# Optimization experiments

Measured on AMD Instinct MI355X. Metric: run time of the kernel, lower is better.

## Reference

```python
import jax, jax.numpy as jnp
import numpy as np

B, S, H = 4, 2048, 1024
NH, HD = 16, 64
ROPE_THETA = 160000.0
SCALE = HD ** -0.5


def _rope_cos_sin(position_ids, dim, theta):
    # neox-style rotary: frequencies over half the head dim
    inv_freq = 1.0 / (theta ** (jnp.arange(0, dim, 2, dtype=jnp.float32) / dim))  # [dim/2]
    freqs = position_ids.astype(jnp.float32)[..., None] * inv_freq  # [B,S,dim/2]
    return jnp.cos(freqs), jnp.sin(freqs)


def _apply_rope(x, cos, sin):
    # x: [B,S,NH,HD]; neox style: rotate halves
    d2 = x.shape[-1] // 2
    x1, x2 = x[..., :d2], x[..., d2:]
    c = cos[:, :, None, :]
    s = sin[:, :, None, :]
    return jnp.concatenate([x1 * c - x2 * s, x2 * c + x1 * s], axis=-1)


def setup_inputs() -> dict:
    key = jax.random.key(0)
    k1, k2, k3 = jax.random.split(key, 3)
    hidden_states = jax.random.normal(k1, (B, S, H), dtype=jnp.float32)
    position_ids = jnp.tile(jnp.arange(S, dtype=jnp.int32)[None, :], (B, 1))
    Wqkv = jax.random.normal(k2, (3 * H, H), dtype=jnp.float32) * (H ** -0.5)
    Wo = jax.random.normal(k3, (H, H), dtype=jnp.float32) * (H ** -0.5)
    return {"hidden_states": hidden_states, "position_ids": position_ids,
            "Wqkv": Wqkv, "Wo": Wo}


def reference(hidden_states, position_ids, Wqkv, Wo):
    # fused QKV projection
    qkv = jnp.einsum('bsh,oh->bso', hidden_states, Wqkv)  # [B,S,3H]
    q, k, v = jnp.split(qkv, 3, axis=-1)
    q = q.reshape(B, S, NH, HD)
    k = k.reshape(B, S, NH, HD)
    v = v.reshape(B, S, NH, HD)
    # rotary embedding (neox style)
    cos, sin = _rope_cos_sin(position_ids, HD, ROPE_THETA)
    q = _apply_rope(q, cos, sin)
    k = _apply_rope(k, cos, sin)
    # full bidirectional (encoder-only, global layer) attention
    scores = jnp.einsum('bqhd,bkhd->bhqk', q, k) * SCALE  # [B,NH,S,S]
    probs = jax.nn.softmax(scores, axis=-1)
    ctx = jnp.einsum('bhqk,bkhd->bqhd', probs, v).reshape(B, S, H)
    # output projection
    return jnp.einsum('bsh,oh->bso', ctx, Wo)
```

## Files before the change

### kernel.cpp

```cpp
#include <hip/hip_runtime.h>
#include <hip/hip_bf16.h>


#define GLOBAL_AS __attribute__((address_space(1)))
#define LDS_AS    __attribute__((address_space(3)))

using f32x4  = __attribute__((ext_vector_type(4))) float;
using f32x16 = __attribute__((ext_vector_type(16))) float;
using s16x8  = __attribute__((ext_vector_type(8))) short;

__device__ __forceinline__ void gld_lds16(const void* g, void* l) {
  __builtin_amdgcn_global_load_lds((const GLOBAL_AS void*)g, (LDS_AS void*)l, 16, 0, 0);
}

__device__ __forceinline__ unsigned short f2bf(float f) {
  unsigned int u = __float_as_uint(f);
  u = (u + 0x7fffu + ((u >> 16) & 1u)) >> 16;
  return (unsigned short)u;
}
__device__ __forceinline__ unsigned int cvt_pk_bf16(float lo, float hi) {
  unsigned int r;
  asm("v_cvt_pk_bf16_f32 %0, %1, %2" : "=v"(r) : "v"(lo), "v"(hi));
  return r;
}
__device__ __forceinline__ void pswap(unsigned int& a, unsigned int& b) {
  asm("v_permlane32_swap_b32 %0, %1" : "+v"(a), "+v"(b));
}

__global__ __launch_bounds__(256) void cvt_all_kernel(const float* __restrict__ h,
                                                      const float* __restrict__ wq,
                                                      const float* __restrict__ wo,
                                                      unsigned short* __restrict__ hb,
                                                      unsigned short* __restrict__ wqb,
                                                      unsigned short* __restrict__ wob) {
  int b = blockIdx.x;
  const float* src; unsigned short* dst; int i;
  if (b < 8192)       { src = h;  dst = hb;  i = b * 256 + threadIdx.x; }
  else if (b < 11264) { src = wq; dst = wqb; i = (b - 8192) * 256 + threadIdx.x; }
  else                { src = wo; dst = wob; i = (b - 11264) * 256 + threadIdx.x; }
  float4 v = ((const float4*)src)[i];
  ushort4 o;
  o.x = f2bf(v.x); o.y = f2bf(v.y); o.z = f2bf(v.z); o.w = f2bf(v.w);
  ((ushort4*)dst)[i] = o;
}

__global__ __launch_bounds__(256) void rope_table_kernel(const int* __restrict__ pos,
                                                         float* __restrict__ ctab,
                                                         float* __restrict__ stab) {
  int idx = blockIdx.x * 256 + threadIdx.x;
  int d = idx & 31;
  int bs = idx >> 5;
  float p = (float)pos[bs];
  float inv = exp2f(-(float)d * 0.5402410118609203f);
  float f = p * inv;
  ctab[idx] = cosf(f);
  stab[idx] = sinf(f);
}

template<int MODE>
__global__ __launch_bounds__(256) void gemm_bt_kernel(const unsigned short* __restrict__ A,
                                                      const unsigned short* __restrict__ Bm,
                                                      void* __restrict__ C, int N, int K,
                                                      const float* __restrict__ ctab,
                                                      const float* __restrict__ stab,
                                                      unsigned short* __restrict__ Qr,
                                                      unsigned short* __restrict__ Kr,
                                                      unsigned short* __restrict__ vbuf) {
  __shared__ char sA[16384];
  __shared__ char sB[16384];
  const int tid  = threadIdx.x;
  const int lane = tid & 63, w = tid >> 6;
  const int g = lane >> 4, c = lane & 15;
  const int wr = w >> 1, wc = w & 1;
  const int m0 = blockIdx.x * 128, n0 = blockIdx.y * 128;
  const char* Ab = (const char*)A;
  const char* Bb = (const char*)Bm;

  f32x4 acc[4][4] = {};
  for (int k0 = 0; k0 < K; k0 += 64) {
    __syncthreads();
#pragma unroll
    for (int rr = 0; rr < 4; ++rr) {
      int o = tid * 16 + rr * 4096;
      int row = o >> 7;
      int col = (o & 127) ^ ((row & 7) << 4);
      gld_lds16(Ab + ((size_t)(m0 + row) * K + k0) * 2 + col, sA + o);
      gld_lds16(Bb + ((size_t)(n0 + row) * K + k0) * 2 + col, sB + o);
    }
    __syncthreads();
#pragma unroll
    for (int ks = 0; ks < 2; ++ks) {
      s16x8 af[4], bfr[4];
#pragma unroll
      for (int i = 0; i < 4; ++i) {
        int row = 64 * wr + 16 * i + c;
        af[i] = *(const s16x8*)(sA + ((row * 128 + ks * 64 + g * 16) ^ ((row & 7) << 4)));
      }
#pragma unroll
      for (int j = 0; j < 4; ++j) {
        int row = 64 * wc + 16 * j + c;
        bfr[j] = *(const s16x8*)(sB + ((row * 128 + ks * 64 + g * 16) ^ ((row & 7) << 4)));
      }
#pragma unroll
      for (int i = 0; i < 4; ++i)
#pragma unroll
        for (int j = 0; j < 4; ++j)
          acc[i][j] = __builtin_amdgcn_mfma_f32_16x16x32_bf16(af[i], bfr[j], acc[i][j], 0, 0, 0);
    }
  }

  if (MODE == 1) {
#pragma unroll
    for (int i = 0; i < 4; ++i)
#pragma unroll
      for (int j = 0; j < 4; ++j)
#pragma unroll
        for (int r = 0; r < 4; ++r) {
          int m = m0 + 64 * wr + 16 * i + 4 * g + r;
          int n = n0 + 64 * wc + 16 * j + c;
          ((float*)C)[(size_t)m * N + n] = acc[i][j][r];
        }
  } else {
    const int t = blockIdx.y;
    if (t < 16) {
      unsigned short* dstb = (t < 8) ? Qr : Kr;
      const float qs = (t < 8) ? 0.18033688011112042f : 1.0f;
      const int h = 2 * (t & 7) + wc;
#pragma unroll
      for (int i = 0; i < 4; ++i)
#pragma unroll
        for (int r = 0; r < 4; ++r) {
          int m = m0 + 64 * wr + 16 * i + 4 * g + r;
          int b = m >> 11, s = m & 2047;
          unsigned short* drow = dstb + ((size_t)(b * 16 + h) * 2048 + s) * 64;
#pragma unroll
          for (int j = 0; j < 2; ++j) {
            int d = 16 * j + c;
            float co = ctab[(size_t)m * 32 + d];
            float si = stab[(size_t)m * 32 + d];
            float x1 = acc[i][j][r], x2 = acc[i][j + 2][r];
            drow[d]      = f2bf((x1 * co - x2 * si) * qs);
            drow[d + 32] = f2bf((x2 * co + x1 * si) * qs);
          }
        }
    } else {
#pragma unroll
      for (int i = 0; i < 4; ++i)
#pragma unroll
        for (int j = 0; j < 4; ++j)
#pragma unroll
          for (int r = 0; r < 4; ++r) {
            int m = m0 + 64 * wr + 16 * i + 4 * g + r;
            int n = (t - 16) * 128 + 64 * wc + 16 * j + c;
            vbuf[(size_t)m * 1024 + n] = f2bf(acc[i][j][r]);
          }
    }
  }
}

__global__ __launch_bounds__(256) void vtrans_kernel(const unsigned short* __restrict__ vbuf,
                                                     unsigned short* __restrict__ Vt) {
  __shared__ unsigned short tile[64][80];
  int bid = blockIdx.x;
  int st = bid & 31, h = (bid >> 5) & 15, b = bid >> 9;
  int s0 = st * 64;
  int t = threadIdx.x;
  {
    int row = t >> 2, part = t & 3;
    const unsigned short* src = vbuf + ((size_t)(b * 2048 + s0 + row)) * 1024 + h * 64 + part * 16;
    uint4 v0 = *(const uint4*)(src);
    uint4 v1 = *(const uint4*)(src + 8);
    *(uint4*)&tile[row][part * 16]     = v0;
    *(uint4*)&tile[row][part * 16 + 8] = v1;
  }
  __syncthreads();
  {
    int d = t >> 2, sp = t & 3;
    unsigned short vals[16];
#pragma unroll
    for (int i = 0; i < 16; ++i) vals[i] = tile[sp * 16 + i][d];
    unsigned short* dst = Vt + ((size_t)(b * 16 + h) * 64 + d) * 2048 + s0 + sp * 16;
    *(uint4*)(dst)     = ((const uint4*)vals)[0];
    *(uint4*)(dst + 8) = ((const uint4*)vals)[1];
  }
}

__global__ __launch_bounds__(256) void attn_kernel(const unsigned short* __restrict__ Q,
                                                   const unsigned short* __restrict__ Kr,
                                                   const unsigned short* __restrict__ Vt,
                                                   unsigned short* __restrict__ Ctx) {
  __shared__ char sK[2][8192];
  __shared__ char sV[2][8192];
  const int tid  = threadIdx.x;
  const int lane = tid & 63, w = tid >> 6;
  const int hi = lane >> 5, ql = lane & 31;
  const int swz = (ql & 7) << 4;
  int lin = blockIdx.x + 16 * blockIdx.y;
  int eff = (lin & 7) * 128 + (lin >> 3);
  const int bh = eff >> 4;
  const int q0 = (eff & 15) * 128;
  const char* kh = (const char*)(Kr + (size_t)bh * 2048 * 64);
  const char* vh = (const char*)(Vt + (size_t)bh * 64 * 2048);

  s16x8 qf[4];
  {
    const char* qrow = (const char*)Q + ((size_t)bh * 2048 + q0 + 32 * w + ql) * 128;
#pragma unroll
    for (int t = 0; t < 4; ++t) qf[t] = *(const s16x8*)(qrow + t * 32 + hi * 16);
  }

#pragma unroll
  for (int rr = 0; rr < 2; ++rr) {
    int o = tid * 16 + rr * 4096;
    int l = o ^ (((o >> 7) & 7) << 4);
    gld_lds16(kh + l, sK[0] + o);
    gld_lds16(vh + (size_t)(o >> 7) * 4096 + (l & 127), sV[0] + o);
  }

  float l_run = 0.f;
  f32x16 oa0 = {}, oa1 = {};

  for (int it = 0; it < 32; ++it) {
    __syncthreads();
    const int cur = it & 1;
    if (it + 1 < 32) {
      int kvn = (it + 1) * 64;
#pragma unroll
      for (int rr = 0; rr < 2; ++rr) {
        int o = tid * 16 + rr * 4096;
        int l = o ^ (((o >> 7) & 7) << 4);
        gld_lds16(kh + (size_t)kvn * 128 + l, sK[cur ^ 1] + o);
        gld_lds16(vh + (size_t)(o >> 7) * 4096 + kvn * 2 + (l & 127), sV[cur ^ 1] + o);
      }
    }

    f32x16 sc0 = {}, sc1 = {};
    __builtin_amdgcn_s_setprio(1);
#pragma unroll
    for (int t = 0; t < 4; ++t) {
      int cx = (t * 32 + hi * 16) ^ swz;
      s16x8 k0 = *(const s16x8*)(sK[cur] + ql * 128 + cx);
      s16x8 k1 = *(const s16x8*)(sK[cur] + (32 + ql) * 128 + cx);
      sc0 = __builtin_amdgcn_mfma_f32_32x32x16_bf16(k0, qf[t], sc0, 0, 0, 0);
      sc1 = __builtin_amdgcn_mfma_f32_32x32x16_bf16(k1, qf[t], sc1, 0, 0, 0);
    }
    __builtin_amdgcn_s_setprio(0);

    float rs = 0.f;
#pragma unroll
    for (int r = 0; r < 16; ++r) { sc0[r] = __builtin_amdgcn_exp2f(sc0[r]); rs += sc0[r]; }
#pragma unroll
    for (int r = 0; r < 16; ++r) { sc1[r] = __builtin_amdgcn_exp2f(sc1[r]); rs += sc1[r]; }
    l_run += rs;

    unsigned int bp[16];
#pragma unroll
    for (int blk = 0; blk < 2; ++blk) {
      const f32x16& s = blk ? sc1 : sc0;
      unsigned int a0 = cvt_pk_bf16(s[0],  s[1]);
      unsigned int a1 = cvt_pk_bf16(s[2],  s[3]);
      unsigned int a2 = cvt_pk_bf16(s[4],  s[5]);
      unsigned int a3 = cvt_pk_bf16(s[6],  s[7]);
      pswap(a0, a2); pswap(a1, a3);
      bp[blk * 8 + 0] = a0; bp[blk * 8 + 1] = a1;
      bp[blk * 8 + 2] = a2; bp[blk * 8 + 3] = a3;
      unsigned int b0 = cvt_pk_bf16(s[8],  s[9]);
      unsigned int b1 = cvt_pk_bf16(s[10], s[11]);
      unsigned int b2 = cvt_pk_bf16(s[12], s[13]);
      unsigned int b3 = cvt_pk_bf16(s[14], s[15]);
      pswap(b0, b2); pswap(b1, b3);
      bp[blk * 8 + 4] = b0; bp[blk * 8 + 5] = b1;
      bp[blk * 8 + 6] = b2; bp[blk * 8 + 7] = b3;
    }

    __builtin_amdgcn_s_setprio(1);
#pragma unroll
    for (int ss = 0; ss < 4; ++ss) {
      uint4 u = {bp[ss * 4], bp[ss * 4 + 1], bp[ss * 4 + 2], bp[ss * 4 + 3]};
      s16x8 pb = __builtin_bit_cast(s16x8, u);
      int cx = (ss * 32 + hi * 16) ^ swz;
      s16x8 v0 = *(const s16x8*)(sV[cur] + ql * 128 + cx);
      s16x8 v1 = *(const s16x8*)(sV[cur] + (32 + ql) * 128 + cx);
      oa0 = __builtin_amdgcn_mfma_f32_32x32x16_bf16(v0, pb, oa0, 0, 0, 0);
      oa1 = __builtin_amdgcn_mfma_f32_32x32x16_bf16(v1, pb, oa1, 0, 0, 0);
    }
    __builtin_amdgcn_s_setprio(0);
  }

  l_run += __shfl_xor(l_run, 32);
  float inv = 1.f / l_run;
  const int b = bh >> 4, h = bh & 15;
  const int q = q0 + 32 * w + ql;
  unsigned short* crow = Ctx + ((size_t)(b * 2048 + q)) * 1024 + h * 64;
#pragma unroll
  for (int dblk = 0; dblk < 2; ++dblk) {
    const f32x16& oa = dblk ? oa1 : oa0;
#pragma unroll
    for (int grp = 0; grp < 4; ++grp) {
      ushort4 st;
      st.x = f2bf(oa[4 * grp + 0] * inv);
      st.y = f2bf(oa[4 * grp + 1] * inv);
      st.z = f2bf(oa[4 * grp + 2] * inv);
      st.w = f2bf(oa[4 * grp + 3] * inv);
      *(ushort4*)(crow + dblk * 32 + 8 * grp + 4 * hi) = st;
    }
  }
}

extern "C" void kernel_launch(void* const* d_in, const int* in_sizes, int n_in,
                              void* d_out, int out_size, void* d_ws, size_t ws_size,
                              hipStream_t stream) {
  const float* hidden = (const float*)d_in[0];
  const int*   pos    = (const int*)d_in[1];
  const float* wqkv   = (const float*)d_in[2];
  const float* wo     = (const float*)d_in[3];

  char* ws = (char*)d_ws;
  unsigned short* hbf  = (unsigned short*)(ws);
  unsigned short* wqbf = (unsigned short*)(ws + 16777216);
  unsigned short* wobf = (unsigned short*)(ws + 23068672);
  unsigned short* vbuf = (unsigned short*)(ws + 25165824);
  unsigned short* Qr   = (unsigned short*)(ws + 41943040);
  unsigned short* Kr   = (unsigned short*)(ws + 58720256);
  unsigned short* Vt   = (unsigned short*)(ws + 75497472);
  unsigned short* ctx  = (unsigned short*)(ws + 92274688);
  float*          ctab = (float*)(ws + 109051904);
  float*          stab = (float*)(ws + 110100480);

  cvt_all_kernel<<<12288, 256, 0, stream>>>(hidden, wqkv, wo, hbf, wqbf, wobf);
  rope_table_kernel<<<1024, 256, 0, stream>>>(pos, ctab, stab);

  dim3 gq(64, 24);
  gemm_bt_kernel<2><<<gq, 256, 0, stream>>>(hbf, wqbf, nullptr, 3072, 1024,
                                            ctab, stab, Qr, Kr, vbuf);

  vtrans_kernel<<<2048, 256, 0, stream>>>(vbuf, Vt);

  dim3 ga(16, 64);
  attn_kernel<<<ga, 256, 0, stream>>>(Qr, Kr, Vt, ctx);

  dim3 go(64, 8);
  gemm_bt_kernel<1><<<go, 256, 0, stream>>>(ctx, wobf, d_out, 1024, 1024,
                                            nullptr, nullptr, nullptr, nullptr, nullptr);
}
```

Baseline: 211.8 us.

## Process two query tiles per wave in attention and deepen K/V prefetch

Each wave now handles 64 query rows (two 32-row tiles) instead of 32, so every K/V fragment read from LDS feeds twice as many MFMAs, and the grid is halved to 512 blocks of 256 queries. The K/V pipeline is restructured to issue loads two iterations ahead with explicit vmcnt waits and raw s_barriers instead of __syncthreads. The aim is to cut LDS read traffic and K/V global reloads per query and to hide load latency better. In exchange, per-thread register use roughly doubles for the score and accumulator tiles, and fewer blocks may reduce occupancy or leave CUs underfilled.

Result: slower. 225.4 us (+6.4%).

```diff
diff --git a/kernel.cpp b/kernel.cpp
--- a/kernel.cpp
+++ b/kernel.cpp
@@ -195,114 +195,143 @@
   const int lane = tid & 63, w = tid >> 6;
   const int hi = lane >> 5, ql = lane & 31;
   const int swz = (ql & 7) << 4;
-  int lin = blockIdx.x + 16 * blockIdx.y;
-  int eff = (lin & 7) * 128 + (lin >> 3);
-  const int bh = eff >> 4;
-  const int q0 = (eff & 15) * 128;
+  int lin = blockIdx.x + 8 * blockIdx.y;
+  int eff = (lin & 7) * 64 + (lin >> 3);
+  const int bh = eff >> 3;
+  const int q0 = (eff & 7) * 256;
   const char* kh = (const char*)(Kr + (size_t)bh * 2048 * 64);
   const char* vh = (const char*)(Vt + (size_t)bh * 64 * 2048);
 
-  s16x8 qf[4];
-  {
-    const char* qrow = (const char*)Q + ((size_t)bh * 2048 + q0 + 32 * w + ql) * 128;
-#pragma unroll
-    for (int t = 0; t < 4; ++t) qf[t] = *(const s16x8*)(qrow + t * 32 + hi * 16);
-  }
-
-#pragma unroll
-  for (int rr = 0; rr < 2; ++rr) {
-    int o = tid * 16 + rr * 4096;
-    int l = o ^ (((o >> 7) & 7) << 4);
-    gld_lds16(kh + l, sK[0] + o);
-    gld_lds16(vh + (size_t)(o >> 7) * 4096 + (l & 127), sV[0] + o);
-  }
-
-  float l_run = 0.f;
-  f32x16 oa0 = {}, oa1 = {};
+  s16x8 qf[2][4];
+#pragma unroll
+  for (int u = 0; u < 2; ++u) {
+    const char* qrow = (const char*)Q + ((size_t)bh * 2048 + q0 + 64 * w + 32 * u + ql) * 128;
+#pragma unroll
+    for (int t = 0; t < 4; ++t) qf[u][t] = *(const s16x8*)(qrow + t * 32 + hi * 16);
+  }
+
+#pragma unroll
+  for (int pt = 0; pt < 2; ++pt) {
+#pragma unroll
+    for (int rr = 0; rr < 2; ++rr) {
+      int o = tid * 16 + rr * 4096;
+      int l = o ^ (((o >> 7) & 7) << 4);
+      gld_lds16(kh + (size_t)pt * 8192 + l, sK[pt] + o);
+      gld_lds16(vh + (size_t)(o >> 7) * 4096 + pt * 128 + (l & 127), sV[pt] + o);
+    }
+  }
+
+  float l_run[2] = {0.f, 0.f};
+  f32x16 oa00 = {}, oa10 = {}, oa01 = {}, oa11 = {};
 
   for (int it = 0; it < 32; ++it) {
-    __syncthreads();
+    if (it < 30) asm volatile("s_waitcnt vmcnt(4)" ::: "memory");
+    else         asm volatile("s_waitcnt vmcnt(0)" ::: "memory");
+    __builtin_amdgcn_sched_barrier(0);
+    __builtin_amdgcn_s_barrier();
+    __builtin_amdgcn_sched_barrier(0);
     const int cur = it & 1;
-    if (it + 1 < 32) {
-      int kvn = (it + 1) * 64;
-#pragma unroll
-      for (int rr = 0; rr < 2; ++rr) {
-        int o = tid * 16 + rr * 4096;
-        int l = o ^ (((o >> 7) & 7) << 4);
-        gld_lds16(kh + (size_t)kvn * 128 + l, sK[cur ^ 1] + o);
-        gld_lds16(vh + (size_t)(o >> 7) * 4096 + kvn * 2 + (l & 127), sV[cur ^ 1] + o);
-      }
-    }
-
-    f32x16 sc0 = {}, sc1 = {};
+
+    f32x16 sc00 = {}, sc01 = {}, sc10 = {}, sc11 = {};
     __builtin_amdgcn_s_setprio(1);
 #pragma unroll
     for (int t = 0; t < 4; ++t) {
       int cx = (t * 32 + hi * 16) ^ swz;
       s16x8 k0 = *(const s16x8*)(sK[cur] + ql * 128 + cx);
       s16x8 k1 = *(const s16x8*)(sK[cur] + (32 + ql) * 128 + cx);
-      sc0 = __builtin_amdgcn_mfma_f32_32x32x16_bf16(k0, qf[t], sc0, 0, 0, 0);
-      sc1 = __builtin_amdgcn_mfma_f32_32x32x16_bf16(k1, qf[t], sc1, 0, 0, 0);
+      sc00 = __builtin_amdgcn_mfma_f32_32x32x16_bf16(k0, qf[0][t], sc00, 0, 0, 0);
+      sc01 = __builtin_amdgcn_mfma_f32_32x32x16_bf16(k1, qf[0][t], sc01, 0, 0, 0);
+      sc10 = __builtin_amdgcn_mfma_f32_32x32x16_bf16(k0, qf[1][t], sc10, 0, 0, 0);
+      sc11 = __builtin_amdgcn_mfma_f32_32x32x16_bf16(k1, qf[1][t], sc11, 0, 0, 0);
     }
     __builtin_amdgcn_s_setprio(0);
 
-    float rs = 0.f;
-#pragma unroll
-    for (int r = 0; r < 16; ++r) { sc0[r] = __builtin_amdgcn_exp2f(sc0[r]); rs += sc0[r]; }
-#pragma unroll
-    for (int r = 0; r < 16; ++r) { sc1[r] = __builtin_amdgcn_exp2f(sc1[r]); rs += sc1[r]; }
-    l_run += rs;
-
-    unsigned int bp[16];
-#pragma unroll
-    for (int blk = 0; blk < 2; ++blk) {
-      const f32x16& s = blk ? sc1 : sc0;
-      unsigned int a0 = cvt_pk_bf16(s[0],  s[1]);
-      unsigned int a1 = cvt_pk_bf16(s[2],  s[3]);
-      unsigned int a2 = cvt_pk_bf16(s[4],  s[5]);
-      unsigned int a3 = cvt_pk_bf16(s[6],  s[7]);
-      pswap(a0, a2); pswap(a1, a3);
-      bp[blk * 8 + 0] = a0; bp[blk * 8 + 1] = a1;
-      bp[blk * 8 + 2] = a2; bp[blk * 8 + 3] = a3;
-      unsigned int b0 = cvt_pk_bf16(s[8],  s[9]);
-      unsigned int b1 = cvt_pk_bf16(s[10], s[11]);
-      unsigned int b2 = cvt_pk_bf16(s[12], s[13]);
-      unsigned int b3 = cvt_pk_bf16(s[14], s[15]);
-      pswap(b0, b2); pswap(b1, b3);
-      bp[blk * 8 + 4] = b0; bp[blk * 8 + 5] = b1;
-      bp[blk * 8 + 6] = b2; bp[blk * 8 + 7] = b3;
+    unsigned int bp0[16], bp1[16];
+#pragma unroll
+    for (int u = 0; u < 2; ++u) {
+      f32x16& s0 = u ? sc10 : sc00;
+      f32x16& s1 = u ? sc11 : sc01;
+      unsigned int* bp = u ? bp1 : bp0;
+      float rs = 0.f;
+#pragma unroll
+      for (int r = 0; r < 16; ++r) { s0[r] = __builtin_amdgcn_exp2f(s0[r]); rs += s0[r]; }
+#pragma unroll
+      for (int r = 0; r < 16; ++r) { s1[r] = __builtin_amdgcn_exp2f(s1[r]); rs += s1[r]; }
+      l_run[u] += rs;
+#pragma unroll
+      for (int blk = 0; blk < 2; ++blk) {
+        const f32x16& s = blk ? s1 : s0;
+        unsigned int a0 = cvt_pk_bf16(s[0],  s[1]);
+        unsigned int a1 = cvt_pk_bf16(s[2],  s[3]);
+        unsigned int a2 = cvt_pk_bf16(s[4],  s[5]);
+        unsigned int a3 = cvt_pk_bf16(s[6],  s[7]);
+        pswap(a0, a2); pswap(a1, a3);
+        bp[blk * 8 + 0] = a0; bp[blk * 8 + 1] = a1;
+        bp[blk * 8 + 2] = a2; bp[blk * 8 + 3] = a3;
+        unsigned int b0 = cvt_pk_bf16(s[8],  s[9]);
+        unsigned int b1 = cvt_pk_bf16(s[10], s[11]);
+        unsigned int b2 = cvt_pk_bf16(s[12], s[13]);
+        unsigned int b3 = cvt_pk_bf16(s[14], s[15]);
+        pswap(b0, b2); pswap(b1, b3);
+        bp[blk * 8 + 4] = b0; bp[blk * 8 + 5] = b1;
+        bp[blk * 8 + 6] = b2; bp[blk * 8 + 7] = b3;
+      }
     }
 
     __builtin_amdgcn_s_setprio(1);
 #pragma unroll
     for (int ss = 0; ss < 4; ++ss) {
-      uint4 u = {bp[ss * 4], bp[ss * 4 + 1], bp[ss * 4 + 2], bp[ss * 4 + 3]};
-      s16x8 pb = __builtin_bit_cast(s16x8, u);
+      uint4 u0 = {bp0[ss * 4], bp0[ss * 4 + 1], bp0[ss * 4 + 2], bp0[ss * 4 + 3]};
+      uint4 u1 = {bp1[ss * 4], bp1[ss * 4 + 1], bp1[ss * 4 + 2], bp1[ss * 4 + 3]};
+      s16x8 pb0 = __builtin_bit_cast(s16x8, u0);
+      s16x8 pb1 = __builtin_bit_cast(s16x8, u1);
       int cx = (ss * 32 + hi * 16) ^ swz;
       s16x8 v0 = *(const s16x8*)(sV[cur] + ql * 128 + cx);
       s16x8 v1 = *(const s16x8*)(sV[cur] + (32 + ql) * 128 + cx);
-      oa0 = __builtin_amdgcn_mfma_f32_32x32x16_bf16(v0, pb, oa0, 0, 0, 0);
-      oa1 = __builtin_amdgcn_mfma_f32_32x32x16_bf16(v1, pb, oa1, 0, 0, 0);
+      oa00 = __builtin_amdgcn_mfma_f32_32x32x16_bf16(v0, pb0, oa00, 0, 0, 0);
+      oa10 = __builtin_amdgcn_mfma_f32_32x32x16_bf16(v1, pb0, oa10, 0, 0, 0);
+      oa01 = __builtin_amdgcn_mfma_f32_32x32x16_bf16(v0, pb1, oa01, 0, 0, 0);
+      oa11 = __builtin_amdgcn_mfma_f32_32x32x16_bf16(v1, pb1, oa11, 0, 0, 0);
     }
     __builtin_amdgcn_s_setprio(0);
-  }
-
-  l_run += __shfl_xor(l_run, 32);
-  float inv = 1.f / l_run;
+
+    __builtin_amdgcn_sched_barrier(0);
+    __builtin_amdgcn_s_barrier();
+    __builtin_amdgcn_sched_barrier(0);
+    if (it + 2 < 32) {
+      int kvn = (it + 2) * 64;
+#pragma unroll
+      for (int rr = 0; rr < 2; ++rr) {
+        int o = tid * 16 + rr * 4096;
+        int l = o ^ (((o >> 7) & 7) << 4);
+        gld_lds16(kh + (size_t)kvn * 128 + l, sK[cur] + o);
+        gld_lds16(vh + (size_t)(o >> 7) * 4096 + kvn * 2 + (l & 127), sV[cur] + o);
+      }
+    }
+  }
+
   const int b = bh >> 4, h = bh & 15;
-  const int q = q0 + 32 * w + ql;
-  unsigned short* crow = Ctx + ((size_t)(b * 2048 + q)) * 1024 + h * 64;
-#pragma unroll
-  for (int dblk = 0; dblk < 2; ++dblk) {
-    const f32x16& oa = dblk ? oa1 : oa0;
-#pragma unroll
-    for (int grp = 0; grp < 4; ++grp) {
-      ushort4 st;
-      st.x = f2bf(oa[4 * grp + 0] * inv);
-      st.y = f2bf(oa[4 * grp + 1] * inv);
-      st.z = f2bf(oa[4 * grp + 2] * inv);
-      st.w = f2bf(oa[4 * grp + 3] * inv);
-      *(ushort4*)(crow + dblk * 32 + 8 * grp + 4 * hi) = st;
+#pragma unroll
+  for (int u = 0; u < 2; ++u) {
+    float l = l_run[u];
+    l += __shfl_xor(l, 32);
+    float inv = 1.f / l;
+    const int q = q0 + 64 * w + 32 * u + ql;
+    unsigned short* crow = Ctx + ((size_t)(b * 2048 + q)) * 1024 + h * 64;
+    const f32x16& o0 = u ? oa01 : oa00;
+    const f32x16& o1 = u ? oa11 : oa10;
+#pragma unroll
+    for (int dblk = 0; dblk < 2; ++dblk) {
+      const f32x16& oa = dblk ? o1 : o0;
+#pragma unroll
+      for (int grp = 0; grp < 4; ++grp) {
+        ushort4 st;
+        st.x = f2bf(oa[4 * grp + 0] * inv);
+        st.y = f2bf(oa[4 * grp + 1] * inv);
+        st.z = f2bf(oa[4 * grp + 2] * inv);
+        st.w = f2bf(oa[4 * grp + 3] * inv);
+        *(ushort4*)(crow + dblk * 32 + 8 * grp + 4 * hi) = st;
+      }
     }
   }
 }
@@ -336,7 +365,7 @@
 
   vtrans_kernel<<<2048, 256, 0, stream>>>(vbuf, Vt);
 
-  dim3 ga(16, 64);
+  dim3 ga(8, 64);
   attn_kernel<<<ga, 256, 0, stream>>>(Qr, Kr, Vt, ctx);
 
   dim3 go(64, 8);
```

## Load K/V fragments directly into registers per wave, dropping LDS staging

Applied to the files above, without the earlier changes.

The attention kernel moves from 256-thread blocks sharing K/V tiles through double-buffered LDS to single-wave blocks that load their own K and V fragments straight from global memory into registers. Each wave prefetches the next iteration's K fragments after the QK MFMAs and the next V fragments after the PV MFMAs, with sched barriers pinning that order. This removes __syncthreads and LDS traffic and allows more independent waves in flight. In exchange, K/V global reads are no longer shared across four waves, so L2/global traffic rises about fourfold and the loads are less coalesced, and more registers are held live.

New measurement: 342.4 us. 61.6% more time.

```diff
diff --git a/kernel.cpp b/kernel.cpp
--- a/kernel.cpp
+++ b/kernel.cpp
@@ -185,66 +185,62 @@
   }
 }
 
-__global__ __launch_bounds__(256) void attn_kernel(const unsigned short* __restrict__ Q,
-                                                   const unsigned short* __restrict__ Kr,
-                                                   const unsigned short* __restrict__ Vt,
-                                                   unsigned short* __restrict__ Ctx) {
-  __shared__ char sK[2][8192];
-  __shared__ char sV[2][8192];
-  const int tid  = threadIdx.x;
-  const int lane = tid & 63, w = tid >> 6;
+__global__ __launch_bounds__(64) void attn_kernel(const unsigned short* __restrict__ Q,
+                                                  const unsigned short* __restrict__ Kr,
+                                                  const unsigned short* __restrict__ Vt,
+                                                  unsigned short* __restrict__ Ctx) {
+  const int lane = threadIdx.x & 63;
   const int hi = lane >> 5, ql = lane & 31;
-  const int swz = (ql & 7) << 4;
-  int lin = blockIdx.x + 16 * blockIdx.y;
-  int eff = (lin & 7) * 128 + (lin >> 3);
-  const int bh = eff >> 4;
-  const int q0 = (eff & 15) * 128;
+  int lin = blockIdx.x;
+  int eff = (lin & 7) * 512 + (lin >> 3);
+  const int bh = eff >> 6;
+  const int q0 = (eff & 63) * 32;
   const char* kh = (const char*)(Kr + (size_t)bh * 2048 * 64);
   const char* vh = (const char*)(Vt + (size_t)bh * 64 * 2048);
 
   s16x8 qf[4];
   {
-    const char* qrow = (const char*)Q + ((size_t)bh * 2048 + q0 + 32 * w + ql) * 128;
+    const char* qrow = (const char*)Q + ((size_t)bh * 2048 + q0 + ql) * 128;
 #pragma unroll
     for (int t = 0; t < 4; ++t) qf[t] = *(const s16x8*)(qrow + t * 32 + hi * 16);
   }
 
-#pragma unroll
-  for (int rr = 0; rr < 2; ++rr) {
-    int o = tid * 16 + rr * 4096;
-    int l = o ^ (((o >> 7) & 7) << 4);
-    gld_lds16(kh + l, sK[0] + o);
-    gld_lds16(vh + (size_t)(o >> 7) * 4096 + (l & 127), sV[0] + o);
+  const char* kb = kh + (size_t)ql * 128 + hi * 16;
+  const char* vb = vh + (size_t)ql * 4096 + hi * 16;
+  s16x8 kf[8], vf[8];
+#pragma unroll
+  for (int t = 0; t < 4; ++t) {
+    kf[2 * t]     = *(const s16x8*)(kb + t * 32);
+    kf[2 * t + 1] = *(const s16x8*)(kb + 32 * 128 + t * 32);
+  }
+#pragma unroll
+  for (int s = 0; s < 4; ++s) {
+    vf[2 * s]     = *(const s16x8*)(vb + s * 32);
+    vf[2 * s + 1] = *(const s16x8*)(vb + 32 * 4096 + s * 32);
   }
 
   float l_run = 0.f;
   f32x16 oa0 = {}, oa1 = {};
 
   for (int it = 0; it < 32; ++it) {
-    __syncthreads();
-    const int cur = it & 1;
-    if (it + 1 < 32) {
-      int kvn = (it + 1) * 64;
-#pragma unroll
-      for (int rr = 0; rr < 2; ++rr) {
-        int o = tid * 16 + rr * 4096;
-        int l = o ^ (((o >> 7) & 7) << 4);
-        gld_lds16(kh + (size_t)kvn * 128 + l, sK[cur ^ 1] + o);
-        gld_lds16(vh + (size_t)(o >> 7) * 4096 + kvn * 2 + (l & 127), sV[cur ^ 1] + o);
-      }
-    }
-
     f32x16 sc0 = {}, sc1 = {};
     __builtin_amdgcn_s_setprio(1);
 #pragma unroll
     for (int t = 0; t < 4; ++t) {
-      int cx = (t * 32 + hi * 16) ^ swz;
-      s16x8 k0 = *(const s16x8*)(sK[cur] + ql * 128 + cx);
-      s16x8 k1 = *(const s16x8*)(sK[cur] + (32 + ql) * 128 + cx);
-      sc0 = __builtin_amdgcn_mfma_f32_32x32x16_bf16(k0, qf[t], sc0, 0, 0, 0);
-      sc1 = __builtin_amdgcn_mfma_f32_32x32x16_bf16(k1, qf[t], sc1, 0, 0, 0);
+      sc0 = __builtin_amdgcn_mfma_f32_32x32x16_bf16(kf[2 * t],     qf[t], sc0, 0, 0, 0);
+      sc1 = __builtin_amdgcn_mfma_f32_32x32x16_bf16(kf[2 * t + 1], qf[t], sc1, 0, 0, 0);
     }
     __builtin_amdgcn_s_setprio(0);
+    __builtin_amdgcn_sched_barrier(0);
+
+    if (it + 1 < 32) {
+      const char* kn = kb + (size_t)(it + 1) * 8192;
+#pragma unroll
+      for (int t = 0; t < 4; ++t) {
+        kf[2 * t]     = *(const s16x8*)(kn + t * 32);
+        kf[2 * t + 1] = *(const s16x8*)(kn + 32 * 128 + t * 32);
+      }
+    }
 
     float rs = 0.f;
 #pragma unroll
@@ -278,19 +274,26 @@
     for (int ss = 0; ss < 4; ++ss) {
       uint4 u = {bp[ss * 4], bp[ss * 4 + 1], bp[ss * 4 + 2], bp[ss * 4 + 3]};
       s16x8 pb = __builtin_bit_cast(s16x8, u);
-      int cx = (ss * 32 + hi * 16) ^ swz;
-      s16x8 v0 = *(const s16x8*)(sV[cur] + ql * 128 + cx);
-      s16x8 v1 = *(const s16x8*)(sV[cur] + (32 + ql) * 128 + cx);
-      oa0 = __builtin_amdgcn_mfma_f32_32x32x16_bf16(v0, pb, oa0, 0, 0, 0);
-      oa1 = __builtin_amdgcn_mfma_f32_32x32x16_bf16(v1, pb, oa1, 0, 0, 0);
+      oa0 = __builtin_amdgcn_mfma_f32_32x32x16_bf16(vf[2 * ss],     pb, oa0, 0, 0, 0);
+      oa1 = __builtin_amdgcn_mfma_f32_32x32x16_bf16(vf[2 * ss + 1], pb, oa1, 0, 0, 0);
     }
     __builtin_amdgcn_s_setprio(0);
+    __builtin_amdgcn_sched_barrier(0);
+
+    if (it + 1 < 32) {
+      const char* vn = vb + (size_t)(it + 1) * 128;
+#pragma unroll
+      for (int s = 0; s < 4; ++s) {
+        vf[2 * s]     = *(const s16x8*)(vn + s * 32);
+        vf[2 * s + 1] = *(const s16x8*)(vn + 32 * 4096 + s * 32);
+      }
+    }
   }
 
   l_run += __shfl_xor(l_run, 32);
   float inv = 1.f / l_run;
   const int b = bh >> 4, h = bh & 15;
-  const int q = q0 + 32 * w + ql;
+  const int q = q0 + ql;
   unsigned short* crow = Ctx + ((size_t)(b * 2048 + q)) * 1024 + h * 64;
 #pragma unroll
   for (int dblk = 0; dblk < 2; ++dblk) {
@@ -336,8 +339,7 @@
 
   vtrans_kernel<<<2048, 256, 0, stream>>>(vbuf, Vt);
 
-  dim3 ga(16, 64);
-  attn_kernel<<<ga, 256, 0, stream>>>(Qr, Kr, Vt, ctx);
+  attn_kernel<<<4096, 64, 0, stream>>>(Qr, Kr, Vt, ctx);
 
   dim3 go(64, 8);
   gemm_bt_kernel<1><<<go, 256, 0, stream>>>(ctx, wobf, d_out, 1024, 1024,
```

## Triple-buffer K/V tiles with prefetch distance two and partial vmcnt waits

Applied to the files above, without the earlier changes.

Replaces the double-buffered K/V LDS staging in the attention kernel with a three-stage ring. Loads are issued two iterations ahead, and the loop waits with vmcnt(4) so that only the older tile's loads must finish before the barrier. The goal is to hide more global-load latency behind the MFMA work. In exchange, LDS per block grows from 32KB to 48KB, which may reduce occupancy, and the hand-written vmcnt counts must stay in step with the number of loads issued per stage.

Result: no change. 215.2 us (+1.6%).

```diff
diff --git a/kernel.cpp b/kernel.cpp
--- a/kernel.cpp
+++ b/kernel.cpp
@@ -189,8 +189,8 @@
                                                    const unsigned short* __restrict__ Kr,
                                                    const unsigned short* __restrict__ Vt,
                                                    unsigned short* __restrict__ Ctx) {
-  __shared__ char sK[2][8192];
-  __shared__ char sV[2][8192];
+  __shared__ char sK[3][8192];
+  __shared__ char sV[3][8192];
   const int tid  = threadIdx.x;
   const int lane = tid & 63, w = tid >> 6;
   const int hi = lane >> 5, ql = lane & 31;
@@ -208,31 +208,40 @@
 #pragma unroll
     for (int t = 0; t < 4; ++t) qf[t] = *(const s16x8*)(qrow + t * 32 + hi * 16);
   }
-
-#pragma unroll
-  for (int rr = 0; rr < 2; ++rr) {
-    int o = tid * 16 + rr * 4096;
-    int l = o ^ (((o >> 7) & 7) << 4);
-    gld_lds16(kh + l, sK[0] + o);
-    gld_lds16(vh + (size_t)(o >> 7) * 4096 + (l & 127), sV[0] + o);
-  }
+  __builtin_amdgcn_sched_barrier(0);
+
+#define STAGE(t, b)                                                              \
+  {                                                                              \
+    _Pragma("unroll")                                                            \
+    for (int rr = 0; rr < 2; ++rr) {                                             \
+      int o = tid * 16 + rr * 4096;                                              \
+      int l = o ^ (((o >> 7) & 7) << 4);                                         \
+      gld_lds16(kh + (size_t)(t) * 8192 + l, sK[b] + o);                         \
+      gld_lds16(vh + (size_t)(o >> 7) * 4096 + (t) * 128 + (l & 127), sV[b] + o);\
+    }                                                                            \
+  }
+
+  STAGE(0, 0);
+  __builtin_amdgcn_sched_barrier(0);
+  STAGE(1, 1);
+  __builtin_amdgcn_sched_barrier(0);
 
   float l_run = 0.f;
   f32x16 oa0 = {}, oa1 = {};
+  int cur = 0;
 
   for (int it = 0; it < 32; ++it) {
-    __syncthreads();
-    const int cur = it & 1;
-    if (it + 1 < 32) {
-      int kvn = (it + 1) * 64;
-#pragma unroll
-      for (int rr = 0; rr < 2; ++rr) {
-        int o = tid * 16 + rr * 4096;
-        int l = o ^ (((o >> 7) & 7) << 4);
-        gld_lds16(kh + (size_t)kvn * 128 + l, sK[cur ^ 1] + o);
-        gld_lds16(vh + (size_t)(o >> 7) * 4096 + kvn * 2 + (l & 127), sV[cur ^ 1] + o);
-      }
-    }
+    if (it == 0 || it == 31) asm volatile("s_waitcnt vmcnt(0)" ::: "memory");
+    else                     asm volatile("s_waitcnt vmcnt(4)" ::: "memory");
+    __builtin_amdgcn_sched_barrier(0);
+    __builtin_amdgcn_s_barrier();
+    __builtin_amdgcn_sched_barrier(0);
+
+    if (it + 2 < 32) {
+      int sb = cur + 2; if (sb >= 3) sb -= 3;
+      STAGE(it + 2, sb);
+    }
+    __builtin_amdgcn_sched_barrier(0);
 
     f32x16 sc0 = {}, sc1 = {};
     __builtin_amdgcn_s_setprio(1);
@@ -285,7 +294,10 @@
       oa1 = __builtin_amdgcn_mfma_f32_32x32x16_bf16(v1, pb, oa1, 0, 0, 0);
     }
     __builtin_amdgcn_s_setprio(0);
-  }
+
+    ++cur; if (cur == 3) cur = 0;
+  }
+#undef STAGE
 
   l_run += __shfl_xor(l_run, 32);
   float inv = 1.f / l_run;
```
